# Kernel optimization log

Hardware: AMD Instinct MI355X
Metric: run time of the kernel (lower is better)

Reference implementation:

```python
import jax, jax.numpy as jnp
import numpy as np

B, S, D = 2, 2048, 1024
H = 16
HD = D // H  # 64
SCALE = HD ** -0.5
EPS = 1e-12  # F.normalize eps


def _rope_sin_cos(length, half, dtype):
    positions = jnp.arange(length, dtype=dtype)
    freqs = jnp.arange(half, dtype=dtype)
    inv_freq = 1.0 / 10000 ** (freqs / max(1, half))
    theta = jnp.einsum('s,f->sf', positions, inv_freq)  # [S, half]
    return jnp.sin(theta)[None, None], jnp.cos(theta)[None, None]  # [1,1,S,half]


def _rotate(x, sin, cos):
    # x: [B,H,S,HD]; interleaved even/odd rotation
    x_even = x[..., 0::2]
    x_odd = x[..., 1::2]
    r_even = x_even * cos - x_odd * sin
    r_odd = x_even * sin + x_odd * cos
    return jnp.stack([r_even, r_odd], axis=-1).reshape(x.shape)


def setup_inputs() -> dict:
    key = jax.random.key(0)
    k1, k2, k3 = jax.random.split(key, 3)
    tokens = jax.random.normal(k1, (B, S, D), dtype=jnp.float32)
    qkv_w = jax.random.normal(k2, (3 * D, D), dtype=jnp.float32) * (D ** -0.5)
    qkv_b = jnp.zeros((3 * D,), dtype=jnp.float32)
    out_w = jax.random.normal(k3, (D, D), dtype=jnp.float32) * (D ** -0.5)
    out_b = jnp.zeros((D,), dtype=jnp.float32)
    return {"tokens": tokens, "qkv_w": qkv_w, "qkv_b": qkv_b,
            "out_w": out_w, "out_b": out_b}


def reference(tokens, qkv_w, qkv_b, out_w, out_b):
    batch, length, _ = tokens.shape
    qkv = tokens @ qkv_w.T + qkv_b                       # [B,S,3D]
    qkv = qkv.reshape(batch, length, 3, H, HD)
    qkv = jnp.transpose(qkv, (0, 3, 1, 2, 4))            # [B,H,S,3,HD]
    q, k, v = qkv[..., 0, :], qkv[..., 1, :], qkv[..., 2, :]
    sin, cos = _rope_sin_cos(length, HD // 2, q.dtype)
    q = _rotate(q, sin, cos)
    k = _rotate(k, sin, cos)
    # QK L2-normalize (F.normalize: x / max(||x||, eps))
    q = q / jnp.maximum(jnp.linalg.norm(q, axis=-1, keepdims=True), EPS)
    k = k / jnp.maximum(jnp.linalg.norm(k, axis=-1, keepdims=True), EPS)
    scores = jnp.einsum('bhqd,bhkd->bhqk', q, k) * SCALE
    attn = jax.nn.softmax(scores, axis=-1)
    out = jnp.einsum('bhqk,bhkd->bhqd', attn, v)          # [B,H,S,HD]
    out = jnp.transpose(out, (0, 2, 1, 3)).reshape(batch, length, D)
    return out @ out_w.T + out_b
```

## Files before the change

### kernel.cpp

```cpp
#include <hip/hip_runtime.h>
#include <hip/hip_bf16.h>
#include <math.h>

#define B_ 2
#define S_ 2048
#define D_ 1024
#define H_ 16
#define HD_ 64
#define BHS (B_*H_*S_)
#define NROWS (B_*S_)

typedef __attribute__((ext_vector_type(8))) short bf16x8;
typedef __attribute__((ext_vector_type(4))) short bf16x4;
typedef __attribute__((ext_vector_type(4))) float f32x4;
typedef __attribute__((ext_vector_type(4))) int i32x4;

#ifdef __HIP_DEVICE_COMPILE__
#define EXP2(x) __builtin_amdgcn_exp2f(x)
#else
#define EXP2(x) exp2f(x)
#endif

#define MFMA32(a, b, c) __builtin_amdgcn_mfma_f32_16x16x32_bf16(a, b, c, 0, 0, 0)

#define SCALE_LOG2E 0.18033688011112043f

#define VMCNT(N) asm volatile("s_waitcnt vmcnt(" #N ")" ::: "memory")
#define SBAR() do { __builtin_amdgcn_s_barrier(); \
                    __builtin_amdgcn_sched_barrier(0); } while (0)

__device__ __forceinline__ short f2bf(float x) {
  __hip_bfloat16 h = __float2bfloat16(x);
  return *reinterpret_cast<short*>(&h);
}
__device__ __forceinline__ int packbf_hu(float lo, float hi) {
  unsigned lb = __float_as_uint(lo) + 0x8000u;
  unsigned hb = __float_as_uint(hi) + 0x8000u;
  return (int)__builtin_amdgcn_perm(hb, lb, 0x07060302u);
}

__device__ __forceinline__ void gload_lds16(const short* g, short* l) {
  __builtin_amdgcn_global_load_lds(
      (const __attribute__((address_space(1))) void*)g,
      (__attribute__((address_space(3))) void*)l, 16, 0, 0);
}

__global__ __launch_bounds__(256) void prep(
    const float* __restrict__ tokens, const float* __restrict__ qkv_w,
    const float* __restrict__ out_w, short* __restrict__ tok_bf,
    short* __restrict__ qkvw_bf, short* __restrict__ outw_bf,
    float* __restrict__ tab) {
  const int i = blockIdx.x * 256 + threadIdx.x;
  const float* src;
  short* dst;
  int j;
  if (i < 524288) {
    src = tokens; dst = tok_bf; j = i;
  } else if (i < 917504) {
    src = qkv_w; dst = qkvw_bf; j = i - 524288;
  } else if (i < 1048576) {
    src = out_w; dst = outw_bf; j = i - 917504;
  } else if (i < 1056768) {
    const int e = (i - 1048576) * 8;
    const int s = e >> 5;
    const int f0 = e & 31;
#pragma unroll
    for (int k = 0; k < 8; k++) {
      const int f = f0 + k;
      const float theta = (float)s * exp2f(-(float)f * 0.41524101186092034f);
      float sn, cs;
      sincosf(theta, &sn, &cs);
      tab[(s * 32 + f) * 2] = sn;
      tab[(s * 32 + f) * 2 + 1] = cs;
    }
    return;
  } else {
    return;
  }
  const float4 a = *(const float4*)(src + (long)j * 8);
  const float4 b = *(const float4*)(src + (long)j * 8 + 4);
  short tmp[8] = {f2bf(a.x), f2bf(a.y), f2bf(a.z), f2bf(a.w),
                  f2bf(b.x), f2bf(b.y), f2bf(b.z), f2bf(b.w)};
  *(bf16x8*)(dst + (long)j * 8) = *(const bf16x8*)tmp;
}

__global__ __launch_bounds__(256) void qkv_mfma(
    const short* __restrict__ A, const short* __restrict__ W,
    const float* __restrict__ bias, const float* __restrict__ tab,
    short* __restrict__ qb, short* __restrict__ kb, short* __restrict__ vtb) {
  __shared__ short smem[24576];
  const int t = threadIdx.x;
  const int w = t >> 6;
  const int lane = t & 63;
  const int col = lane & 15;
  const int quad = lane >> 4;
  const int wm = w >> 1;
  const int wn = w & 1;
  const int bid = blockIdx.x;
  const int xcd = bid & 7;
  const int seq = bid >> 3;
  const int m0 = (seq / 3) * 128;
  const int n0 = (xcd * 3 + seq % 3) * 128;

  f32x4 acc[4][4] = {};

  auto stage = [&](short* As, short* Bs, int k0) {
#pragma unroll
    for (int i = 0; i < 2; i++) {
      const int c0 = i * 256 + w * 64;
      const int c = c0 + lane;
      const int row = c >> 2;
      const int gseg = (c & 3) ^ ((row >> 1) & 3);
      gload_lds16(&A[(m0 + row) * 1024 + k0 + gseg * 8], As + c0 * 8);
    }
#pragma unroll
    for (int i = 0; i < 2; i++) {
      const int c0 = i * 256 + w * 64;
      const int c = c0 + lane;
      const int row = c >> 2;
      const int gseg = (c & 3) ^ ((row >> 1) & 3);
      gload_lds16(&W[(n0 + row) * 1024 + k0 + gseg * 8], Bs + c0 * 8);
    }
  };

  auto compute = [&](const short* As, const short* Bs) {
    bf16x8 af[4], bfr[4];
#pragma unroll
    for (int mt = 0; mt < 4; mt++) {
      const int m = wm * 64 + mt * 16 + col;
      af[mt] = *(const bf16x8*)&As[m * 32 + ((quad ^ ((m >> 1) & 3)) * 8)];
    }
#pragma unroll
    for (int nt = 0; nt < 4; nt++) {
      const int n = wn * 64 + nt * 16 + col;
      bfr[nt] = *(const bf16x8*)&Bs[n * 32 + ((quad ^ ((n >> 1) & 3)) * 8)];
    }
#pragma unroll
    for (int mt = 0; mt < 4; mt++)
#pragma unroll
      for (int nt = 0; nt < 4; nt++)
        acc[mt][nt] = MFMA32(af[mt], bfr[nt], acc[mt][nt]);
  };

  short* As0 = smem;          short* Bs0 = smem + 4096;
  short* As1 = smem + 8192;   short* Bs1 = smem + 12288;
  short* As2 = smem + 16384;  short* Bs2 = smem + 20480;

  stage(As0, Bs0, 0);
  stage(As1, Bs1, 32);
  for (int it = 0; it < 10; it++) {
    const int k = it * 96;
    VMCNT(4); SBAR(); stage(As2, Bs2, k + 64);  compute(As0, Bs0);
    VMCNT(4); SBAR(); stage(As0, Bs0, k + 96);  compute(As1, Bs1);
    VMCNT(4); SBAR(); stage(As1, Bs1, k + 128); compute(As2, Bs2);
  }
  VMCNT(4); SBAR(); compute(As0, Bs0);
  VMCNT(0); SBAR(); compute(As1, Bs1);
  __syncthreads();

  const int j_base = n0 + wn * 64;
  const int c = j_base >> 10;
  const int h = (j_base >> 6) & 15;
  float bi[4];
#pragma unroll
  for (int nt = 0; nt < 4; nt++) bi[nt] = bias[j_base + nt * 16 + col];

  if (c < 2) {
    short* dst = (c == 0) ? qb : kb;
    float* Tf = (float*)smem + w * 1088;
#pragma unroll
    for (int mt = 0; mt < 4; mt++) {
#pragma unroll
      for (int nt = 0; nt < 4; nt++)
#pragma unroll
        for (int r = 0; r < 4; r++)
          Tf[(quad * 4 + r) * 68 + nt * 16 + col] = acc[mt][nt][r] + bi[nt];
#pragma unroll
      for (int p = 0; p < 4; p++) {
        const int rloc = p * 4 + quad;
        const int n = m0 + wm * 64 + mt * 16 + rloc;
        const int bidx = n >> 11;
        const int s = n & 2047;
        const float4 xv = *(const float4*)&Tf[rloc * 68 + col * 4];
        const float4 tc = *(const float4*)&tab[s * 64 + col * 4];
        const float e0 = xv.x * tc.y - xv.y * tc.x;
        const float o0 = xv.x * tc.x + xv.y * tc.y;
        const float e1 = xv.z * tc.w - xv.w * tc.z;
        const float o1 = xv.z * tc.z + xv.w * tc.w;
        float ss = e0 * e0 + o0 * o0 + e1 * e1 + o1 * o1;
        ss += __shfl_xor(ss, 1, 64);
        ss += __shfl_xor(ss, 2, 64);
        ss += __shfl_xor(ss, 4, 64);
        ss += __shfl_xor(ss, 8, 64);
        float scl = 1.0f / fmaxf(sqrtf(ss), 1e-12f);
        if (c == 0) scl *= SCALE_LOG2E;
        int2 pk;
        pk.x = packbf_hu(e0 * scl, o0 * scl);
        pk.y = packbf_hu(e1 * scl, o1 * scl);
        *(int2*)&dst[((long)(bidx * 16 + h) * 2048 + s) * 64 + col * 4] = pk;
      }
    }
  } else {
    const int bidx = m0 >> 11;
    const int st = ((m0 & 2047) >> 6) + wm;
    short* vbase = vtb + ((long)(bidx * 16 + h) * 32 + st) * 4096;
#pragma unroll
    for (int mtp = 0; mtp < 2; mtp++)
#pragma unroll
      for (int ntq = 0; ntq < 4; ntq++) {
        int4 pk4;
        pk4.x = packbf_hu(acc[2 * mtp][ntq][0] + bi[ntq],
                          acc[2 * mtp][ntq][1] + bi[ntq]);
        pk4.y = packbf_hu(acc[2 * mtp][ntq][2] + bi[ntq],
                          acc[2 * mtp][ntq][3] + bi[ntq]);
        pk4.z = packbf_hu(acc[2 * mtp + 1][ntq][0] + bi[ntq],
                          acc[2 * mtp + 1][ntq][1] + bi[ntq]);
        pk4.w = packbf_hu(acc[2 * mtp + 1][ntq][2] + bi[ntq],
                          acc[2 * mtp + 1][ntq][3] + bi[ntq]);
        *(int4*)&vbase[(mtp * 4 + ntq) * 512 + quad * 128 + col * 8] = pk4;
      }
  }
}

__global__ __launch_bounds__(512) void attn_mfma(
    const short* __restrict__ qb,
    const short* __restrict__ kb,
    const short* __restrict__ vt,
    short* __restrict__ ob) {
  __shared__ __align__(16) char smem[65536];
  short* Ks = (short*)smem;
  short* Vs = Ks + 16384;
  const int t = threadIdx.x;
  const int w = t >> 6;
  const int grp = w >> 2;
  const int wl = w & 3;
  const int lane = t & 63;
  const int col = lane & 15;
  const int quad = lane >> 4;
  const int bh = blockIdx.x;
  const int q0 = blockIdx.y * 128;
  const long hb = (long)bh * S_ * 64;
  const short* kg = kb + hb;
  const short* vg = vt + (long)bh * 64 * S_;

  bf16x8 qa[2][2];
#pragma unroll
  for (int mt2 = 0; mt2 < 2; mt2++)
#pragma unroll
    for (int h = 0; h < 2; h++)
      qa[mt2][h] = *(const bf16x8*)&qb[hb +
          (long)(q0 + wl * 32 + mt2 * 16 + col) * 64 + h * 32 + quad * 8];

  const int tt = (wl << 6) | lane;
  int kofs[2];
#pragma unroll
  for (int i = 0; i < 2; i++) {
    const int cc = tt + 256 * i;
    kofs[i] = ((cc >> 7) * 16 + (cc & 15)) * 64 + ((cc >> 6) & 1) * 32 +
              ((cc >> 4) & 3) * 8;
  }

  short* KfL0 = Ks + grp * 4096;
  short* KfL1 = KfL0 + 8192;
  short* VfL0 = Vs + grp * 4096;
  short* VfL1 = VfL0 + 8192;

  f32x4 oacc[2][4] = {};
  f32x4 lacc[2] = {};
  const short oneb = 0x3F80;
  const bf16x8 ones8 = {oneb, oneb, oneb, oneb, oneb, oneb, oneb, oneb};

  auto stage = [&](short* KfL, short* VfL, int kt) {
    const short* kgp = kg + (long)kt * 64;
    const short* vgp = vg + (long)(kt >> 6) * 4096;
#pragma unroll
    for (int i = 0; i < 2; i++) {
      gload_lds16(kgp + kofs[i], KfL + i * 2048 + wl * 512);
      gload_lds16(vgp + (tt + 256 * i) * 8, VfL + i * 2048 + wl * 512);
    }
  };

  auto compute = [&](const short* KfL, const short* VfL) {
#pragma unroll
    for (int ntp = 0; ntp < 2; ntp++) {
      i32x4 pw[2];
#pragma unroll
      for (int half = 0; half < 2; half++) {
        const int nt = ntp * 2 + half;
        const bf16x8 ka0 =
            *(const bf16x8*)&KfL[nt * 1024 + quad * 128 + col * 8];
        const bf16x8 ka1 =
            *(const bf16x8*)&KfL[nt * 1024 + 512 + quad * 128 + col * 8];
#pragma unroll
        for (int mt2 = 0; mt2 < 2; mt2++) {
          f32x4 z = {0.f, 0.f, 0.f, 0.f};
          z = MFMA32(ka0, qa[mt2][0], z);
          z = MFMA32(ka1, qa[mt2][1], z);
          const float e0 = EXP2(z[0]);
          const float e1 = EXP2(z[1]);
          const float e2 = EXP2(z[2]);
          const float e3 = EXP2(z[3]);
          if (half == 0) {
            pw[mt2].x = packbf_hu(e0, e1);
            pw[mt2].y = packbf_hu(e2, e3);
          } else {
            pw[mt2].z = packbf_hu(e0, e1);
            pw[mt2].w = packbf_hu(e2, e3);
          }
        }
      }
      const bf16x8 pb0 = __builtin_bit_cast(bf16x8, pw[0]);
      const bf16x8 pb1 = __builtin_bit_cast(bf16x8, pw[1]);
      lacc[0] = MFMA32(ones8, pb0, lacc[0]);
      lacc[1] = MFMA32(ones8, pb1, lacc[1]);
#pragma unroll
      for (int dt = 0; dt < 4; dt++) {
        const bf16x8 va = *(const bf16x8*)
            &VfL[(ntp * 4 + dt) * 512 + quad * 128 + col * 8];
        oacc[0][dt] = MFMA32(va, pb0, oacc[0][dt]);
        oacc[1][dt] = MFMA32(va, pb1, oacc[1][dt]);
      }
    }
  };

  const int base = grp * 1024;
  stage(KfL0, VfL0, base);
  __syncthreads();
  for (int it = 0; it < 8; it++) {
    const int kt0 = base + it * 128;
    stage(KfL1, VfL1, kt0 + 64);
    compute(KfL0, VfL0);
    __syncthreads();
    if (it < 7) stage(KfL0, VfL0, kt0 + 128);
    compute(KfL1, VfL1);
    __syncthreads();
  }

  float* Ocomb = (float*)smem;
  float* lsumC = (float*)(smem + 34816);
  if (grp == 1) {
#pragma unroll
    for (int mt2 = 0; mt2 < 2; mt2++) {
      const int qloc = wl * 32 + mt2 * 16 + col;
      if (quad == 0) lsumC[qloc] = lacc[mt2][0];
#pragma unroll
      for (int dt = 0; dt < 4; dt++)
        *(f32x4*)&Ocomb[qloc * 68 + dt * 16 + quad * 4] = oacc[mt2][dt];
    }
  }
  __syncthreads();
  if (grp == 0) {
#pragma unroll
    for (int mt2 = 0; mt2 < 2; mt2++) {
      const int qloc = wl * 32 + mt2 * 16 + col;
      const float inv = 1.0f / (lacc[mt2][0] + lsumC[qloc]);
      short* orow = ob + hb + (long)(q0 + qloc) * 64;
#pragma unroll
      for (int dt = 0; dt < 4; dt++) {
        const float4 oc = *(const float4*)&Ocomb[qloc * 68 + dt * 16 + quad * 4];
        int2 pk;
        pk.x = packbf_hu((oacc[mt2][dt][0] + oc.x) * inv,
                         (oacc[mt2][dt][1] + oc.y) * inv);
        pk.y = packbf_hu((oacc[mt2][dt][2] + oc.z) * inv,
                         (oacc[mt2][dt][3] + oc.w) * inv);
        *(int2*)&orow[dt * 16 + quad * 4] = pk;
      }
    }
  }
}

__global__ __launch_bounds__(256) void out_mfma(
    const short* __restrict__ O, const short* __restrict__ W,
    const float* __restrict__ bias, float* __restrict__ out) {
  __shared__ short smem[12288];
  const int t = threadIdx.x;
  const int w = t >> 6;
  const int lane = t & 63;
  const int col = lane & 15;
  const int quad = lane >> 4;
  const int wm = w >> 1;
  const int wn = w & 1;
  const int bid = blockIdx.x;
  const int xcd = bid & 7;
  const int seq = bid >> 3;
  const int m0 = (seq >> 1) * 64;
  const int n0 = (xcd * 2 + (seq & 1)) * 64;

  f32x4 acc[2][2] = {};

  auto stage = [&](short* As, short* Bs, int k0) {
    {
      const int c = w * 64 + lane;
      const int row = c >> 2;
      const int gseg = (c & 3) ^ ((row >> 1) & 3);
      const int n = m0 + row;
      const int bidx = n >> 11;
      const int s = n & 2047;
      const int kk = k0 + gseg * 8;
      gload_lds16(&O[((long)(bidx * 16 + (kk >> 6)) * 2048 + s) * 64 + (kk & 63)],
                  As + w * 512);
    }
    {
      const int c = w * 64 + lane;
      const int row = c >> 2;
      const int gseg = (c & 3) ^ ((row >> 1) & 3);
      gload_lds16(&W[(n0 + row) * 1024 + k0 + gseg * 8], Bs + w * 512);
    }
  };

  auto compute = [&](const short* As, const short* Bs) {
    bf16x8 af[2], bfr[2];
#pragma unroll
    for (int mt = 0; mt < 2; mt++) {
      const int m = wm * 32 + mt * 16 + col;
      af[mt] = *(const bf16x8*)&As[m * 32 + ((quad ^ ((m >> 1) & 3)) * 8)];
    }
#pragma unroll
    for (int nt = 0; nt < 2; nt++) {
      const int n = wn * 32 + nt * 16 + col;
      bfr[nt] = *(const bf16x8*)&Bs[n * 32 + ((quad ^ ((n >> 1) & 3)) * 8)];
    }
#pragma unroll
    for (int mt = 0; mt < 2; mt++)
#pragma unroll
      for (int nt = 0; nt < 2; nt++)
        acc[mt][nt] = MFMA32(af[mt], bfr[nt], acc[mt][nt]);
  };

  short* As0 = smem;          short* Bs0 = smem + 2048;
  short* As1 = smem + 4096;   short* Bs1 = smem + 6144;
  short* As2 = smem + 8192;   short* Bs2 = smem + 10240;

  stage(As0, Bs0, 0);
  stage(As1, Bs1, 32);
  for (int it = 0; it < 10; it++) {
    const int k = it * 96;
    VMCNT(2); SBAR(); stage(As2, Bs2, k + 64);  compute(As0, Bs0);
    VMCNT(2); SBAR(); stage(As0, Bs0, k + 96);  compute(As1, Bs1);
    VMCNT(2); SBAR(); stage(As1, Bs1, k + 128); compute(As2, Bs2);
  }
  VMCNT(2); SBAR(); compute(As0, Bs0);
  VMCNT(0); SBAR(); compute(As1, Bs1);

  float bi[2];
#pragma unroll
  for (int nt = 0; nt < 2; nt++) bi[nt] = bias[n0 + wn * 32 + nt * 16 + col];
#pragma unroll
  for (int mt = 0; mt < 2; mt++) {
#pragma unroll
    for (int r = 0; r < 4; r++) {
      const int n = m0 + wm * 32 + mt * 16 + quad * 4 + r;
#pragma unroll
      for (int nt = 0; nt < 2; nt++)
        out[(long)n * 1024 + n0 + wn * 32 + nt * 16 + col] =
            acc[mt][nt][r] + bi[nt];
    }
  }
}

extern "C" void kernel_launch(void* const* d_in, const int* in_sizes, int n_in,
                              void* d_out, int out_size, void* d_ws,
                              size_t ws_size, hipStream_t stream) {
  const float* tokens = (const float*)d_in[0];
  const float* qkv_w = (const float*)d_in[1];
  const float* qkv_b = (const float*)d_in[2];
  const float* out_w = (const float*)d_in[3];
  const float* out_b = (const float*)d_in[4];
  float* out = (float*)d_out;

  const size_t per = (size_t)BHS * HD_;
  float* tab = (float*)d_ws;
  short* tok_bf = (short*)(tab + 2048 * 64);
  short* qkvw_bf = tok_bf + per;
  short* outw_bf = qkvw_bf + 3 * per / 4;
  short* q_bf = outw_bf + per / 4;
  short* k_bf = q_bf + per;
  short* vt_bf = k_bf + per;
  short* O_bf = vt_bf + per;

  hipLaunchKernelGGL(prep, dim3(4128), dim3(256), 0, stream, tokens, qkv_w,
                     out_w, tok_bf, qkvw_bf, outw_bf, tab);
  hipLaunchKernelGGL(qkv_mfma, dim3(768), dim3(256), 0, stream, tok_bf,
                     qkvw_bf, qkv_b, tab, q_bf, k_bf, vt_bf);
  hipLaunchKernelGGL(attn_mfma, dim3(B_ * H_, S_ / 128), dim3(512), 0, stream,
                     q_bf, k_bf, vt_bf, O_bf);
  hipLaunchKernelGGL(out_mfma, dim3(1024), dim3(256), 0, stream, O_bf,
                     outw_bf, out_b, out);
}
```

Measured before the change: 180.8 us.

## Widen GEMM K-tiles to 64 with double buffering and halve attention waves

Both projection GEMMs now stage 64-wide K tiles with a new 8-way XOR swizzle and use a two-buffer pipeline with explicit vmcnt waits and barriers, replacing the three-buffer 32-wide scheme. The attention kernel drops from 8 to 4 waves per block, so each wave handles 64 query rows instead of 32 and reuses each loaded K/V fragment across more MFMAs. Its loop switches from __syncthreads to explicit waitcnt plus barrier with scheduling fences. The aim is fewer barriers per K step and more MFMA work per LDS read, at the cost of more registers and less latency hiding in attention.

```diff
diff --git a/kernel.cpp b/kernel.cpp
--- a/kernel.cpp
+++ b/kernel.cpp
@@ -28,6 +28,7 @@
 #define VMCNT(N) asm volatile("s_waitcnt vmcnt(" #N ")" ::: "memory")
 #define SBAR() do { __builtin_amdgcn_s_barrier(); \
                     __builtin_amdgcn_sched_barrier(0); } while (0)
+#define SCHED0() __builtin_amdgcn_sched_barrier(0)
 
 __device__ __forceinline__ short f2bf(float x) {
   __hip_bfloat16 h = __float2bfloat16(x);
@@ -88,7 +89,7 @@
     const short* __restrict__ A, const short* __restrict__ W,
     const float* __restrict__ bias, const float* __restrict__ tab,
     short* __restrict__ qb, short* __restrict__ kb, short* __restrict__ vtb) {
-  __shared__ short smem[24576];
+  __shared__ short smem[32768];
   const int t = threadIdx.x;
   const int w = t >> 6;
   const int lane = t & 63;
@@ -106,56 +107,62 @@
 
   auto stage = [&](short* As, short* Bs, int k0) {
 #pragma unroll
-    for (int i = 0; i < 2; i++) {
+    for (int i = 0; i < 4; i++) {
       const int c0 = i * 256 + w * 64;
       const int c = c0 + lane;
-      const int row = c >> 2;
-      const int gseg = (c & 3) ^ ((row >> 1) & 3);
+      const int row = c >> 3;
+      const int gseg = (c & 7) ^ (row & 7);
       gload_lds16(&A[(m0 + row) * 1024 + k0 + gseg * 8], As + c0 * 8);
     }
 #pragma unroll
-    for (int i = 0; i < 2; i++) {
+    for (int i = 0; i < 4; i++) {
       const int c0 = i * 256 + w * 64;
       const int c = c0 + lane;
-      const int row = c >> 2;
-      const int gseg = (c & 3) ^ ((row >> 1) & 3);
+      const int row = c >> 3;
+      const int gseg = (c & 7) ^ (row & 7);
       gload_lds16(&W[(n0 + row) * 1024 + k0 + gseg * 8], Bs + c0 * 8);
     }
   };
 
   auto compute = [&](const short* As, const short* Bs) {
-    bf16x8 af[4], bfr[4];
-#pragma unroll
-    for (int mt = 0; mt < 4; mt++) {
-      const int m = wm * 64 + mt * 16 + col;
-      af[mt] = *(const bf16x8*)&As[m * 32 + ((quad ^ ((m >> 1) & 3)) * 8)];
-    }
-#pragma unroll
-    for (int nt = 0; nt < 4; nt++) {
-      const int n = wn * 64 + nt * 16 + col;
-      bfr[nt] = *(const bf16x8*)&Bs[n * 32 + ((quad ^ ((n >> 1) & 3)) * 8)];
-    }
-#pragma unroll
-    for (int mt = 0; mt < 4; mt++)
-#pragma unroll
-      for (int nt = 0; nt < 4; nt++)
-        acc[mt][nt] = MFMA32(af[mt], bfr[nt], acc[mt][nt]);
+#pragma unroll
+    for (int half = 0; half < 2; half++) {
+      bf16x8 af[4], bfr[4];
+#pragma unroll
+      for (int mt = 0; mt < 4; mt++) {
+        const int m = wm * 64 + mt * 16 + col;
+        af[mt] =
+            *(const bf16x8*)&As[m * 64 + (((quad + half * 4) ^ (m & 7)) * 8)];
+      }
+#pragma unroll
+      for (int nt = 0; nt < 4; nt++) {
+        const int n = wn * 64 + nt * 16 + col;
+        bfr[nt] =
+            *(const bf16x8*)&Bs[n * 64 + (((quad + half * 4) ^ (n & 7)) * 8)];
+      }
+#pragma unroll
+      for (int mt = 0; mt < 4; mt++)
+#pragma unroll
+        for (int nt = 0; nt < 4; nt++)
+          acc[mt][nt] = MFMA32(af[mt], bfr[nt], acc[mt][nt]);
+    }
   };
 
-  short* As0 = smem;          short* Bs0 = smem + 4096;
-  short* As1 = smem + 8192;   short* Bs1 = smem + 12288;
-  short* As2 = smem + 16384;  short* Bs2 = smem + 20480;
+  short* As0 = smem;          short* Bs0 = smem + 8192;
+  short* As1 = smem + 16384;  short* Bs1 = smem + 24576;
 
   stage(As0, Bs0, 0);
-  stage(As1, Bs1, 32);
-  for (int it = 0; it < 10; it++) {
-    const int k = it * 96;
-    VMCNT(4); SBAR(); stage(As2, Bs2, k + 64);  compute(As0, Bs0);
-    VMCNT(4); SBAR(); stage(As0, Bs0, k + 96);  compute(As1, Bs1);
-    VMCNT(4); SBAR(); stage(As1, Bs1, k + 128); compute(As2, Bs2);
-  }
-  VMCNT(4); SBAR(); compute(As0, Bs0);
-  VMCNT(0); SBAR(); compute(As1, Bs1);
+  for (int it = 0; it < 8; it++) {
+    const int k = it * 128;
+    VMCNT(0); SBAR();
+    stage(As1, Bs1, k + 64);
+    SCHED0();
+    compute(As0, Bs0);
+    VMCNT(0); SBAR();
+    if (it < 7) stage(As0, Bs0, k + 128);
+    SCHED0();
+    compute(As1, Bs1);
+  }
   __syncthreads();
 
   const int j_base = n0 + wn * 64;
@@ -222,7 +229,7 @@
   }
 }
 
-__global__ __launch_bounds__(512) void attn_mfma(
+__global__ __launch_bounds__(256) void attn_mfma(
     const short* __restrict__ qb,
     const short* __restrict__ kb,
     const short* __restrict__ vt,
@@ -232,8 +239,8 @@
   short* Vs = Ks + 16384;
   const int t = threadIdx.x;
   const int w = t >> 6;
-  const int grp = w >> 2;
-  const int wl = w & 3;
+  const int grp = w >> 1;
+  const int wl = w & 1;
   const int lane = t & 63;
   const int col = lane & 15;
   const int quad = lane >> 4;
@@ -243,19 +250,19 @@
   const short* kg = kb + hb;
   const short* vg = vt + (long)bh * 64 * S_;
 
-  bf16x8 qa[2][2];
-#pragma unroll
-  for (int mt2 = 0; mt2 < 2; mt2++)
+  bf16x8 qa[4][2];
+#pragma unroll
+  for (int mt2 = 0; mt2 < 4; mt2++)
 #pragma unroll
     for (int h = 0; h < 2; h++)
       qa[mt2][h] = *(const bf16x8*)&qb[hb +
-          (long)(q0 + wl * 32 + mt2 * 16 + col) * 64 + h * 32 + quad * 8];
+          (long)(q0 + wl * 64 + mt2 * 16 + col) * 64 + h * 32 + quad * 8];
 
   const int tt = (wl << 6) | lane;
-  int kofs[2];
-#pragma unroll
-  for (int i = 0; i < 2; i++) {
-    const int cc = tt + 256 * i;
+  int kofs[4];
+#pragma unroll
+  for (int i = 0; i < 4; i++) {
+    const int cc = i * 128 + tt;
     kofs[i] = ((cc >> 7) * 16 + (cc & 15)) * 64 + ((cc >> 6) & 1) * 32 +
               ((cc >> 4) & 3) * 8;
   }
@@ -265,8 +272,8 @@
   short* VfL0 = Vs + grp * 4096;
   short* VfL1 = VfL0 + 8192;
 
-  f32x4 oacc[2][4] = {};
-  f32x4 lacc[2] = {};
+  f32x4 oacc[4][4] = {};
+  f32x4 lacc[4] = {};
   const short oneb = 0x3F80;
   const bf16x8 ones8 = {oneb, oneb, oneb, oneb, oneb, oneb, oneb, oneb};
 
@@ -274,16 +281,16 @@
     const short* kgp = kg + (long)kt * 64;
     const short* vgp = vg + (long)(kt >> 6) * 4096;
 #pragma unroll
-    for (int i = 0; i < 2; i++) {
-      gload_lds16(kgp + kofs[i], KfL + i * 2048 + wl * 512);
-      gload_lds16(vgp + (tt + 256 * i) * 8, VfL + i * 2048 + wl * 512);
+    for (int i = 0; i < 4; i++) {
+      gload_lds16(kgp + kofs[i], KfL + i * 1024 + wl * 512);
+      gload_lds16(vgp + (i * 128 + tt) * 8, VfL + i * 1024 + wl * 512);
     }
   };
 
   auto compute = [&](const short* KfL, const short* VfL) {
 #pragma unroll
     for (int ntp = 0; ntp < 2; ntp++) {
-      i32x4 pw[2];
+      i32x4 pw[4];
 #pragma unroll
       for (int half = 0; half < 2; half++) {
         const int nt = ntp * 2 + half;
@@ -292,7 +299,7 @@
         const bf16x8 ka1 =
             *(const bf16x8*)&KfL[nt * 1024 + 512 + quad * 128 + col * 8];
 #pragma unroll
-        for (int mt2 = 0; mt2 < 2; mt2++) {
+        for (int mt2 = 0; mt2 < 4; mt2++) {
           f32x4 z = {0.f, 0.f, 0.f, 0.f};
           z = MFMA32(ka0, qa[mt2][0], z);
           z = MFMA32(ka1, qa[mt2][1], z);
@@ -309,39 +316,44 @@
           }
         }
       }
-      const bf16x8 pb0 = __builtin_bit_cast(bf16x8, pw[0]);
-      const bf16x8 pb1 = __builtin_bit_cast(bf16x8, pw[1]);
-      lacc[0] = MFMA32(ones8, pb0, lacc[0]);
-      lacc[1] = MFMA32(ones8, pb1, lacc[1]);
+      bf16x8 pb[4];
+#pragma unroll
+      for (int j = 0; j < 4; j++) {
+        pb[j] = __builtin_bit_cast(bf16x8, pw[j]);
+        lacc[j] = MFMA32(ones8, pb[j], lacc[j]);
+      }
 #pragma unroll
       for (int dt = 0; dt < 4; dt++) {
         const bf16x8 va = *(const bf16x8*)
             &VfL[(ntp * 4 + dt) * 512 + quad * 128 + col * 8];
-        oacc[0][dt] = MFMA32(va, pb0, oacc[0][dt]);
-        oacc[1][dt] = MFMA32(va, pb1, oacc[1][dt]);
+#pragma unroll
+        for (int j = 0; j < 4; j++)
+          oacc[j][dt] = MFMA32(va, pb[j], oacc[j][dt]);
       }
     }
   };
 
   const int base = grp * 1024;
   stage(KfL0, VfL0, base);
-  __syncthreads();
   for (int it = 0; it < 8; it++) {
     const int kt0 = base + it * 128;
+    VMCNT(0); SBAR();
     stage(KfL1, VfL1, kt0 + 64);
+    SCHED0();
     compute(KfL0, VfL0);
-    __syncthreads();
+    VMCNT(0); SBAR();
     if (it < 7) stage(KfL0, VfL0, kt0 + 128);
+    SCHED0();
     compute(KfL1, VfL1);
-    __syncthreads();
-  }
+  }
+  __syncthreads();
 
   float* Ocomb = (float*)smem;
   float* lsumC = (float*)(smem + 34816);
   if (grp == 1) {
 #pragma unroll
-    for (int mt2 = 0; mt2 < 2; mt2++) {
-      const int qloc = wl * 32 + mt2 * 16 + col;
+    for (int mt2 = 0; mt2 < 4; mt2++) {
+      const int qloc = wl * 64 + mt2 * 16 + col;
       if (quad == 0) lsumC[qloc] = lacc[mt2][0];
 #pragma unroll
       for (int dt = 0; dt < 4; dt++)
@@ -351,8 +363,8 @@
   __syncthreads();
   if (grp == 0) {
 #pragma unroll
-    for (int mt2 = 0; mt2 < 2; mt2++) {
-      const int qloc = wl * 32 + mt2 * 16 + col;
+    for (int mt2 = 0; mt2 < 4; mt2++) {
+      const int qloc = wl * 64 + mt2 * 16 + col;
       const float inv = 1.0f / (lacc[mt2][0] + lsumC[qloc]);
       short* orow = ob + hb + (long)(q0 + qloc) * 64;
 #pragma unroll
@@ -372,7 +384,7 @@
 __global__ __launch_bounds__(256) void out_mfma(
     const short* __restrict__ O, const short* __restrict__ W,
     const float* __restrict__ bias, float* __restrict__ out) {
-  __shared__ short smem[12288];
+  __shared__ short smem[16384];
   const int t = threadIdx.x;
   const int w = t >> 6;
   const int lane = t & 63;
@@ -389,58 +401,68 @@
   f32x4 acc[2][2] = {};
 
   auto stage = [&](short* As, short* Bs, int k0) {
-    {
-      const int c = w * 64 + lane;
-      const int row = c >> 2;
-      const int gseg = (c & 3) ^ ((row >> 1) & 3);
+#pragma unroll
+    for (int i = 0; i < 2; i++) {
+      const int c0 = i * 256 + w * 64;
+      const int c = c0 + lane;
+      const int row = c >> 3;
+      const int gseg = (c & 7) ^ (row & 7);
       const int n = m0 + row;
       const int bidx = n >> 11;
       const int s = n & 2047;
       const int kk = k0 + gseg * 8;
       gload_lds16(&O[((long)(bidx * 16 + (kk >> 6)) * 2048 + s) * 64 + (kk & 63)],
-                  As + w * 512);
-    }
-    {
-      const int c = w * 64 + lane;
-      const int row = c >> 2;
-      const int gseg = (c & 3) ^ ((row >> 1) & 3);
-      gload_lds16(&W[(n0 + row) * 1024 + k0 + gseg * 8], Bs + w * 512);
+                  As + c0 * 8);
+    }
+#pragma unroll
+    for (int i = 0; i < 2; i++) {
+      const int c0 = i * 256 + w * 64;
+      const int c = c0 + lane;
+      const int row = c >> 3;
+      const int gseg = (c & 7) ^ (row & 7);
+      gload_lds16(&W[(n0 + row) * 1024 + k0 + gseg * 8], Bs + c0 * 8);
     }
   };
 
   auto compute = [&](const short* As, const short* Bs) {
-    bf16x8 af[2], bfr[2];
-#pragma unroll
-    for (int mt = 0; mt < 2; mt++) {
-      const int m = wm * 32 + mt * 16 + col;
-      af[mt] = *(const bf16x8*)&As[m * 32 + ((quad ^ ((m >> 1) & 3)) * 8)];
-    }
-#pragma unroll
-    for (int nt = 0; nt < 2; nt++) {
-      const int n = wn * 32 + nt * 16 + col;
-      bfr[nt] = *(const bf16x8*)&Bs[n * 32 + ((quad ^ ((n >> 1) & 3)) * 8)];
-    }
-#pragma unroll
-    for (int mt = 0; mt < 2; mt++)
-#pragma unroll
-      for (int nt = 0; nt < 2; nt++)
-        acc[mt][nt] = MFMA32(af[mt], bfr[nt], acc[mt][nt]);
+#pragma unroll
+    for (int half = 0; half < 2; half++) {
+      bf16x8 af[2], bfr[2];
+#pragma unroll
+      for (int mt = 0; mt < 2; mt++) {
+        const int m = wm * 32 + mt * 16 + col;
+        af[mt] =
+            *(const bf16x8*)&As[m * 64 + (((quad + half * 4) ^ (m & 7)) * 8)];
+      }
+#pragma unroll
+      for (int nt = 0; nt < 2; nt++) {
+        const int n = wn * 32 + nt * 16 + col;
+        bfr[nt] =
+            *(const bf16x8*)&Bs[n * 64 + (((quad + half * 4) ^ (n & 7)) * 8)];
+      }
+#pragma unroll
+      for (int mt = 0; mt < 2; mt++)
+#pragma unroll
+        for (int nt = 0; nt < 2; nt++)
+          acc[mt][nt] = MFMA32(af[mt], bfr[nt], acc[mt][nt]);
+    }
   };
 
-  short* As0 = smem;          short* Bs0 = smem + 2048;
-  short* As1 = smem + 4096;   short* Bs1 = smem + 6144;
-  short* As2 = smem + 8192;   short* Bs2 = smem + 10240;
+  short* As0 = smem;         short* Bs0 = smem + 4096;
+  short* As1 = smem + 8192;  short* Bs1 = smem + 12288;
 
   stage(As0, Bs0, 0);
-  stage(As1, Bs1, 32);
-  for (int it = 0; it < 10; it++) {
-    const int k = it * 96;
-    VMCNT(2); SBAR(); stage(As2, Bs2, k + 64);  compute(As0, Bs0);
-    VMCNT(2); SBAR(); stage(As0, Bs0, k + 96);  compute(As1, Bs1);
-    VMCNT(2); SBAR(); stage(As1, Bs1, k + 128); compute(As2, Bs2);
-  }
-  VMCNT(2); SBAR(); compute(As0, Bs0);
-  VMCNT(0); SBAR(); compute(As1, Bs1);
+  for (int it = 0; it < 8; it++) {
+    const int k = it * 128;
+    VMCNT(0); SBAR();
+    stage(As1, Bs1, k + 64);
+    SCHED0();
+    compute(As0, Bs0);
+    VMCNT(0); SBAR();
+    if (it < 7) stage(As0, Bs0, k + 128);
+    SCHED0();
+    compute(As1, Bs1);
+  }
 
   float bi[2];
 #pragma unroll
@@ -482,7 +504,7 @@
                      out_w, tok_bf, qkvw_bf, outw_bf, tab);
   hipLaunchKernelGGL(qkv_mfma, dim3(768), dim3(256), 0, stream, tok_bf,
                      qkvw_bf, qkv_b, tab, q_bf, k_bf, vt_bf);
-  hipLaunchKernelGGL(attn_mfma, dim3(B_ * H_, S_ / 128), dim3(512), 0, stream,
+  hipLaunchKernelGGL(attn_mfma, dim3(B_ * H_, S_ / 128), dim3(256), 0, stream,
                      q_bf, k_bf, vt_bf, O_bf);
   hipLaunchKernelGGL(out_mfma, dim3(1024), dim3(256), 0, stream, O_bf,
                      outw_bf, out_b, out);
```

After: 196.2 us. 8.6% more time.
